# Optimization experiments

Measured on AMD Instinct MI355X. Metric: run time of the kernel, lower is better.

Reference implementation:

```python
import jax, jax.numpy as jnp
from jax import lax
import numpy as np


def setup_inputs() -> dict:
    key = jax.random.key(0)
    ks = jax.random.split(key, 9)
    B, T, H = 64, 4096, 128
    G = 4 * H
    s = 1.0 / np.sqrt(H)  # PyTorch LSTM default init scale
    return {
        "data": jax.random.normal(ks[0], (B, T, 1), dtype=jnp.float32),
        "h0": jax.random.normal(ks[1], (B, H), dtype=jnp.float32),
        "c0": jax.random.normal(ks[2], (B, H), dtype=jnp.float32),
        "W_ih": jax.random.uniform(ks[3], (G, 1), jnp.float32, -s, s),
        "W_hh": jax.random.uniform(ks[4], (G, H), jnp.float32, -s, s),
        "b_ih": jax.random.uniform(ks[5], (G,), jnp.float32, -s, s),
        "b_hh": jax.random.uniform(ks[6], (G,), jnp.float32, -s, s),
        "W_out": jax.random.uniform(ks[7], (1, H), jnp.float32, -s, s),
        "b_out": jax.random.uniform(ks[8], (1,), jnp.float32, -s, s),
    }


def reference(data, h0, c0, W_ih, W_hh, b_ih, b_hh, W_out, b_out):
    # Single-layer batch-first LSTM (PyTorch gate order i,f,g,o), then Linear on last step.
    H = h0.shape[-1]
    # Precompute input projections for all timesteps: [B, T, 4H] -> time-major [T, B, 4H]
    x_proj = jnp.einsum("bti,gi->btg", data, W_ih) + b_ih + b_hh
    x_proj = jnp.swapaxes(x_proj, 0, 1)

    def step(carry, xg):
        h, c = carry
        gates = xg + h @ W_hh.T  # [B, 4H]
        i = jax.nn.sigmoid(gates[:, 0 * H:1 * H])
        f = jax.nn.sigmoid(gates[:, 1 * H:2 * H])
        g = jnp.tanh(gates[:, 2 * H:3 * H])
        o = jax.nn.sigmoid(gates[:, 3 * H:4 * H])
        c = f * c + i * g
        h = o * jnp.tanh(c)
        return (h, c), None

    (hT, _), _ = lax.scan(step, (h0, c0), x_proj)
    # out[:, -1, :] of the LSTM is hT; final linear projection -> [B, 1]
    return hT @ W_out.T + b_out
```

## Files before the change

kernel.cpp:

```cpp
#include <hip/hip_runtime.h>
#include <math.h>

constexpr int Hdim = 128;
constexpr int TMAX = 4096;

typedef _Float16 v8h __attribute__((ext_vector_type(8)));
typedef float v4f __attribute__((ext_vector_type(4)));

#if __has_builtin(__builtin_amdgcn_exp2f)
__device__ __forceinline__ float exp2_fast(float x) {
  return __builtin_amdgcn_exp2f(x);
}
#else
__device__ __forceinline__ float exp2_fast(float x) {
  return __expf(x * 0.6931471805599453f);
}
#endif

__device__ __forceinline__ float sel4(v4f d, int r) {
  const float s01 = (r & 1) ? d.y : d.x;
  const float s23 = (r & 1) ? d.w : d.z;
  return (r & 2) ? s23 : s01;
}

__global__ __launch_bounds__(512) void lstm_mfma(
    const float* __restrict__ data, const float* __restrict__ h0,
    const float* __restrict__ c0, const float* __restrict__ W_ih,
    const float* __restrict__ W_hh, const float* __restrict__ b_ih,
    const float* __restrict__ b_hh, const float* __restrict__ W_out,
    const float* __restrict__ b_out, float* __restrict__ out, int T) {
  __shared__ __align__(16) float xs[TMAX];
  __shared__ __align__(16) _Float16 hbuf[2][Hdim];

  const int b = blockIdx.x;
  const int tid = threadIdx.x;
  const int lane = tid & 63;
  const int wv = tid >> 6;
  const int p = lane >> 4;
  const int m = lane & 15;
  const int r = m & 3;
  const int el = 16 * wv + 4 * p + r;

  {
    const float4* src = (const float4*)(data + (size_t)b * T);
    float4* dst = (float4*)xs;
    for (int i = tid; i < T / 4; i += 512) dst[i] = src[i];
  }

  constexpr float L2E = 1.44269504088896f;

  v8h a[4][4];
#pragma unroll
  for (int g = 0; g < 4; ++g) {
    const int row = 128 * g + 16 * wv + m;
    const float Mr = (g == 2) ? 2.0f * L2E : -L2E;
    const float* wr = W_hh + (size_t)row * Hdim + 8 * p;
#pragma unroll
    for (int c = 0; c < 4; ++c) {
      float4 v0 = ((const float4*)(wr + 32 * c))[0];
      float4 v1 = ((const float4*)(wr + 32 * c))[1];
      a[g][c] = v8h{(_Float16)(Mr * v0.x), (_Float16)(Mr * v0.y),
                    (_Float16)(Mr * v0.z), (_Float16)(Mr * v0.w),
                    (_Float16)(Mr * v1.x), (_Float16)(Mr * v1.y),
                    (_Float16)(Mr * v1.z), (_Float16)(Mr * v1.w)};
    }
  }

  float wih[4], bs[4];
#pragma unroll
  for (int g = 0; g < 4; ++g) {
    const float Mr = (g == 2) ? 2.0f * L2E : -L2E;
    const int row = 128 * g + el;
    wih[g] = Mr * W_ih[row];
    bs[g] = Mr * (b_ih[row] + b_hh[row]);
  }

  float cst = c0[(size_t)b * Hdim + el];
  if (tid < 128) hbuf[0][tid] = (_Float16)h0[(size_t)b * Hdim + tid];
  __syncthreads();

#pragma unroll 2
  for (int t = 0; t < T; ++t) {
    const _Float16* hb = hbuf[t & 1];
    v8h bq[4];
#pragma unroll
    for (int c = 0; c < 4; ++c) bq[c] = *(const v8h*)(hb + 32 * c + 8 * p);
    const float xt = xs[t];

    v4f d[4];
#pragma unroll
    for (int g = 0; g < 4; ++g) {
      v4f acc = {0.f, 0.f, 0.f, 0.f};
#pragma unroll
      for (int c = 0; c < 4; ++c)
        acc = __builtin_amdgcn_mfma_f32_16x16x32_f16(a[g][c], bq[c], acc,
                                                     0, 0, 0);
      d[g] = acc;
    }

    const float zi = sel4(d[0], r);
    const float zf = sel4(d[1], r);
    const float zg = sel4(d[2], r);
    const float zo = sel4(d[3], r);

    const float yi =
        __builtin_amdgcn_rcpf(1.0f + exp2_fast(fmaf(xt, wih[0], bs[0]) + zi));
    const float yf =
        __builtin_amdgcn_rcpf(1.0f + exp2_fast(fmaf(xt, wih[1], bs[1]) + zf));
    const float yg = fmaf(
        -2.0f,
        __builtin_amdgcn_rcpf(1.0f + exp2_fast(fmaf(xt, wih[2], bs[2]) + zg)),
        1.0f);
    const float yo =
        __builtin_amdgcn_rcpf(1.0f + exp2_fast(fmaf(xt, wih[3], bs[3]) + zo));

    cst = fmaf(yf, cst, yi * yg);
    const float th = fmaf(
        -2.0f, __builtin_amdgcn_rcpf(1.0f + exp2_fast(cst * (2.0f * L2E))),
        1.0f);
    const float h = yo * th;

    if (m < 4) hbuf[(t + 1) & 1][el] = (_Float16)h;
    __syncthreads();
  }

  if (tid < 64) {
    const _Float16* hf = hbuf[T & 1];
    float sum =
        (float)hf[tid] * W_out[tid] + (float)hf[tid + 64] * W_out[tid + 64];
#pragma unroll
    for (int off = 32; off > 0; off >>= 1) sum += __shfl_down(sum, off, 64);
    if (tid == 0) out[b] = sum + b_out[0];
  }
}

extern "C" void kernel_launch(void* const* d_in, const int* in_sizes, int n_in,
                              void* d_out, int out_size, void* d_ws,
                              size_t ws_size, hipStream_t stream) {
  const float* data = (const float*)d_in[0];
  const float* h0 = (const float*)d_in[1];
  const float* c0 = (const float*)d_in[2];
  const float* W_ih = (const float*)d_in[3];
  const float* W_hh = (const float*)d_in[4];
  const float* b_ih = (const float*)d_in[5];
  const float* b_hh = (const float*)d_in[6];
  const float* W_out = (const float*)d_in[7];
  const float* b_out = (const float*)d_in[8];
  float* out = (float*)d_out;

  const int B = in_sizes[1] / Hdim;
  const int T = in_sizes[0] / B;

  lstm_mfma<<<B, 512, 0, stream>>>(data, h0, c0, W_ih, W_hh, b_ih, b_hh,
                                   W_out, b_out, out, T);
}
```

Baseline: 1.885 ms.

## Split hidden units between MFMA waves and packed-dot VALU waves

Waves 0-3 keep the MFMA path for hidden units 0-63. Waves 4-7 now compute hidden units 64-127 with fdot2 packed-fp16 dot products, where each group of four lanes covers one unit and combines partials and gate activations through DPP shuffles. The goal is to spread the per-step recurrent matvec across the matrix and vector pipes, so the serial critical path per timestep gets shorter. The cost is divergent code between waves, extra DPP reduction latency on the VALU half, and an imbalance that can leave the slower half setting the pace at each barrier.

Result: slower. 2.342 ms (+24.2%).

```diff
diff --git a/kernel.cpp b/kernel.cpp
--- a/kernel.cpp
+++ b/kernel.cpp
@@ -5,7 +5,14 @@
 constexpr int TMAX = 4096;
 
 typedef _Float16 v8h __attribute__((ext_vector_type(8)));
+typedef _Float16 v2h __attribute__((ext_vector_type(2)));
 typedef float v4f __attribute__((ext_vector_type(4)));
+
+template <int CTRL>
+__device__ __forceinline__ float dppf(float v) {
+  return __int_as_float(
+      __builtin_amdgcn_update_dpp(0, __float_as_int(v), CTRL, 0xF, 0xF, true));
+}
 
 #if __has_builtin(__builtin_amdgcn_exp2f)
 __device__ __forceinline__ float exp2_fast(float x) {
@@ -23,7 +30,11 @@
   return (r & 2) ? s23 : s01;
 }
 
-__global__ __launch_bounds__(512) void lstm_mfma(
+__device__ __forceinline__ v2h get2(v8h v, int i) {
+  return v2h{v[2 * i], v[2 * i + 1]};
+}
+
+__global__ __launch_bounds__(512) void lstm_hybrid(
     const float* __restrict__ data, const float* __restrict__ h0,
     const float* __restrict__ c0, const float* __restrict__ W_ih,
     const float* __restrict__ W_hh, const float* __restrict__ b_ih,
@@ -36,10 +47,14 @@
   const int tid = threadIdx.x;
   const int lane = tid & 63;
   const int wv = tid >> 6;
+  const bool mf = (wv < 4);
+
   const int p = lane >> 4;
   const int m = lane & 15;
   const int r = m & 3;
-  const int el = 16 * wv + 4 * p + r;
+  const int q = lane & 3;
+
+  const int el = mf ? (16 * wv + 4 * p + r) : (64 + 16 * (wv - 4) + (lane >> 2));
 
   {
     const float4* src = (const float4*)(data + (size_t)b * T);
@@ -49,31 +64,61 @@
 
   constexpr float L2E = 1.44269504088896f;
 
-  v8h a[4][4];
-#pragma unroll
-  for (int g = 0; g < 4; ++g) {
-    const int row = 128 * g + 16 * wv + m;
-    const float Mr = (g == 2) ? 2.0f * L2E : -L2E;
-    const float* wr = W_hh + (size_t)row * Hdim + 8 * p;
-#pragma unroll
-    for (int c = 0; c < 4; ++c) {
-      float4 v0 = ((const float4*)(wr + 32 * c))[0];
-      float4 v1 = ((const float4*)(wr + 32 * c))[1];
-      a[g][c] = v8h{(_Float16)(Mr * v0.x), (_Float16)(Mr * v0.y),
-                    (_Float16)(Mr * v0.z), (_Float16)(Mr * v0.w),
-                    (_Float16)(Mr * v1.x), (_Float16)(Mr * v1.y),
-                    (_Float16)(Mr * v1.z), (_Float16)(Mr * v1.w)};
+  v8h A[4][4];
+  if (mf) {
+#pragma unroll
+    for (int g = 0; g < 4; ++g) {
+      const int row = 128 * g + 16 * wv + m;
+      const float Mr = (g == 2) ? 2.0f * L2E : -L2E;
+      const float* wr = W_hh + (size_t)row * Hdim + 8 * p;
+#pragma unroll
+      for (int c = 0; c < 4; ++c) {
+        float4 v0 = ((const float4*)(wr + 32 * c))[0];
+        float4 v1 = ((const float4*)(wr + 32 * c))[1];
+        A[g][c] = v8h{(_Float16)(Mr * v0.x), (_Float16)(Mr * v0.y),
+                      (_Float16)(Mr * v0.z), (_Float16)(Mr * v0.w),
+                      (_Float16)(Mr * v1.x), (_Float16)(Mr * v1.y),
+                      (_Float16)(Mr * v1.z), (_Float16)(Mr * v1.w)};
+      }
+    }
+  } else {
+#pragma unroll
+    for (int g = 0; g < 4; ++g) {
+      const int row = 128 * g + el;
+      const float Mr = (g == 2) ? 2.0f * L2E : -L2E;
+      const float* wr = W_hh + (size_t)row * Hdim + 32 * q;
+#pragma unroll
+      for (int c = 0; c < 4; ++c) {
+        float4 v0 = ((const float4*)(wr + 8 * c))[0];
+        float4 v1 = ((const float4*)(wr + 8 * c))[1];
+        A[g][c] = v8h{(_Float16)(Mr * v0.x), (_Float16)(Mr * v0.y),
+                      (_Float16)(Mr * v0.z), (_Float16)(Mr * v0.w),
+                      (_Float16)(Mr * v1.x), (_Float16)(Mr * v1.y),
+                      (_Float16)(Mr * v1.z), (_Float16)(Mr * v1.w)};
+      }
     }
   }
 
   float wih[4], bs[4];
-#pragma unroll
-  for (int g = 0; g < 4; ++g) {
-    const float Mr = (g == 2) ? 2.0f * L2E : -L2E;
-    const int row = 128 * g + el;
-    wih[g] = Mr * W_ih[row];
-    bs[g] = Mr * (b_ih[row] + b_hh[row]);
-  }
+  float As = 1.0f, Bs = 0.0f;
+  if (mf) {
+#pragma unroll
+    for (int g = 0; g < 4; ++g) {
+      const float Mr = (g == 2) ? 2.0f * L2E : -L2E;
+      const int row = 128 * g + el;
+      wih[g] = Mr * W_ih[row];
+      bs[g] = Mr * (b_ih[row] + b_hh[row]);
+    }
+  } else {
+    const int row = 128 * q + el;
+    const float MkL = (q == 2) ? 2.0f * L2E : -L2E;
+    wih[0] = MkL * W_ih[row];
+    bs[0] = MkL * (b_ih[row] + b_hh[row]);
+    As = (q == 2) ? -2.0f : 1.0f;
+    Bs = (q == 2) ? 1.0f : 0.0f;
+  }
+  const bool qb0 = (q & 1) != 0;
+  const bool qb1 = (q & 2) != 0;
 
   float cst = c0[(size_t)b * Hdim + el];
   if (tid < 128) hbuf[0][tid] = (_Float16)h0[(size_t)b * Hdim + tid];
@@ -82,45 +127,93 @@
 #pragma unroll 2
   for (int t = 0; t < T; ++t) {
     const _Float16* hb = hbuf[t & 1];
-    v8h bq[4];
-#pragma unroll
-    for (int c = 0; c < 4; ++c) bq[c] = *(const v8h*)(hb + 32 * c + 8 * p);
     const float xt = xs[t];
-
-    v4f d[4];
-#pragma unroll
-    for (int g = 0; g < 4; ++g) {
-      v4f acc = {0.f, 0.f, 0.f, 0.f};
-#pragma unroll
-      for (int c = 0; c < 4; ++c)
-        acc = __builtin_amdgcn_mfma_f32_16x16x32_f16(a[g][c], bq[c], acc,
-                                                     0, 0, 0);
-      d[g] = acc;
-    }
-
-    const float zi = sel4(d[0], r);
-    const float zf = sel4(d[1], r);
-    const float zg = sel4(d[2], r);
-    const float zo = sel4(d[3], r);
-
-    const float yi =
-        __builtin_amdgcn_rcpf(1.0f + exp2_fast(fmaf(xt, wih[0], bs[0]) + zi));
-    const float yf =
-        __builtin_amdgcn_rcpf(1.0f + exp2_fast(fmaf(xt, wih[1], bs[1]) + zf));
-    const float yg = fmaf(
-        -2.0f,
-        __builtin_amdgcn_rcpf(1.0f + exp2_fast(fmaf(xt, wih[2], bs[2]) + zg)),
-        1.0f);
-    const float yo =
-        __builtin_amdgcn_rcpf(1.0f + exp2_fast(fmaf(xt, wih[3], bs[3]) + zo));
-
-    cst = fmaf(yf, cst, yi * yg);
-    const float th = fmaf(
-        -2.0f, __builtin_amdgcn_rcpf(1.0f + exp2_fast(cst * (2.0f * L2E))),
-        1.0f);
-    const float h = yo * th;
-
-    if (m < 4) hbuf[(t + 1) & 1][el] = (_Float16)h;
+    float hnew;
+
+    if (mf) {
+      v8h bq[4];
+#pragma unroll
+      for (int c = 0; c < 4; ++c) bq[c] = *(const v8h*)(hb + 32 * c + 8 * p);
+
+      v4f d[4];
+#pragma unroll
+      for (int g = 0; g < 4; ++g) {
+        v4f acc = {0.f, 0.f, 0.f, 0.f};
+#pragma unroll
+        for (int c = 0; c < 4; ++c)
+          acc = __builtin_amdgcn_mfma_f32_16x16x32_f16(A[g][c], bq[c], acc,
+                                                       0, 0, 0);
+        d[g] = acc;
+      }
+
+      const float zi = sel4(d[0], r);
+      const float zf = sel4(d[1], r);
+      const float zg = sel4(d[2], r);
+      const float zo = sel4(d[3], r);
+
+      const float yi = __builtin_amdgcn_rcpf(
+          1.0f + exp2_fast(fmaf(xt, wih[0], bs[0]) + zi));
+      const float yf = __builtin_amdgcn_rcpf(
+          1.0f + exp2_fast(fmaf(xt, wih[1], bs[1]) + zf));
+      const float yg =
+          fmaf(-2.0f,
+               __builtin_amdgcn_rcpf(
+                   1.0f + exp2_fast(fmaf(xt, wih[2], bs[2]) + zg)),
+               1.0f);
+      const float yo = __builtin_amdgcn_rcpf(
+          1.0f + exp2_fast(fmaf(xt, wih[3], bs[3]) + zo));
+
+      cst = fmaf(yf, cst, yi * yg);
+      const float th = fmaf(
+          -2.0f, __builtin_amdgcn_rcpf(1.0f + exp2_fast(cst * (2.0f * L2E))),
+          1.0f);
+      hnew = yo * th;
+    } else {
+      v8h hx[4];
+#pragma unroll
+      for (int c = 0; c < 4; ++c) hx[c] = *(const v8h*)(hb + 32 * q + 8 * c);
+
+      float a0 = 0.f, a1 = 0.f, a2 = 0.f, a3 = 0.f;
+#pragma unroll
+      for (int c = 0; c < 4; ++c) {
+#pragma unroll
+        for (int jj = 0; jj < 4; ++jj) {
+          const v2h hp2 = get2(hx[c], jj);
+          a0 = __builtin_amdgcn_fdot2(get2(A[0][c], jj), hp2, a0, false);
+          a1 = __builtin_amdgcn_fdot2(get2(A[1][c], jj), hp2, a1, false);
+          a2 = __builtin_amdgcn_fdot2(get2(A[2][c], jj), hp2, a2, false);
+          a3 = __builtin_amdgcn_fdot2(get2(A[3][c], jj), hp2, a3, false);
+        }
+      }
+
+      float x01 = qb0 ? a1 : a0;
+      float y01 = qb0 ? a0 : a1;
+      x01 += dppf<0xB1>(y01);
+      float x23 = qb0 ? a3 : a2;
+      float y23 = qb0 ? a2 : a3;
+      x23 += dppf<0xB1>(y23);
+      float z = qb1 ? x23 : x01;
+      float zz = qb1 ? x01 : x23;
+      z += dppf<0x4E>(zz);
+
+      const float pre = fmaf(xt, wih[0], bs[0]) + z;
+      const float y =
+          fmaf(As, __builtin_amdgcn_rcpf(1.0f + exp2_fast(pre)), Bs);
+
+      const float yi = dppf<0x00>(y);
+      const float yf = dppf<0x55>(y);
+      const float yg = dppf<0xAA>(y);
+      const float yo = dppf<0xFF>(y);
+
+      cst = fmaf(yf, cst, yi * yg);
+      const float th = fmaf(
+          -2.0f, __builtin_amdgcn_rcpf(1.0f + exp2_fast(cst * (2.0f * L2E))),
+          1.0f);
+      hnew = yo * th;
+    }
+
+    const bool writer = mf ? (m < 4) : (q == 0);
+    if (writer) hbuf[(t + 1) & 1][el] = (_Float16)hnew;
     __syncthreads();
   }
 
@@ -151,6 +244,6 @@
   const int B = in_sizes[1] / Hdim;
   const int T = in_sizes[0] / B;
 
-  lstm_mfma<<<B, 512, 0, stream>>>(data, h0, c0, W_ih, W_hh, b_ih, b_hh,
-                                   W_out, b_out, out, T);
-}
+  lstm_hybrid<<<B, 512, 0, stream>>>(data, h0, c0, W_ih, W_hh, b_ih, b_hh,
+                                     W_out, b_out, out, T);
+}
```
